# Performance work log

Measured on AMD Instinct MI355X. Metric: run time of the kernel, lower is better.

The kernel has to match this reference:

```python
import jax, jax.numpy as jnp
import numpy as np

B, N, D = 512, 2048, 128
MASK_NEG = 1e30


def setup_inputs() -> dict:
    key = jax.random.key(0)
    ks = jax.random.split(key, 8)
    Q = jax.random.normal(ks[0], (B, D), dtype=jnp.float32)
    K = jax.random.normal(ks[1], (B, N, D), dtype=jnp.float32)
    V = jax.random.normal(ks[2], (B, N, D), dtype=jnp.float32)
    adj = jax.random.randint(ks[3], (B, N), 0, 2).astype(jnp.float32)  # 0/1 mask
    s_mask = jnp.zeros((B, N), dtype=jnp.int32)  # unused by forward, kept for fidelity
    # nn.Linear params (PyTorch default uniform init scale)
    bound = 1.0 / np.sqrt(D)
    W1 = jax.random.uniform(ks[4], (D, D), minval=-bound, maxval=bound, dtype=jnp.float32)
    b1 = jax.random.uniform(ks[5], (D,), minval=-bound, maxval=bound, dtype=jnp.float32)
    W2 = jax.random.uniform(ks[6], (D, D), minval=-bound, maxval=bound, dtype=jnp.float32)
    b2 = jax.random.uniform(ks[7], (D,), minval=-bound, maxval=bound, dtype=jnp.float32)
    return {"Q": Q, "K": K, "V": V, "adj": adj, "s_mask": s_mask,
            "W1": W1, "b1": b1, "W2": W2, "b2": b2}


def reference(Q, K, V, adj, s_mask, W1, b1, W2, b2):
    # linear1(Q): (B, D); linear2(K): (B, N, D)  (torch Linear: x @ W.T + b)
    Qp = Q @ W1.T + b1
    Kp = jnp.einsum('bnd,de->bne', K, W2.T) + b2
    # bmm(K, Q.unsqueeze(2)).permute -> (B, 1, N) attention logits
    alpha = jnp.einsum('bnd,bd->bn', Kp, Qp)
    alpha = alpha - (1.0 - adj) * 1e30  # mask_logic with adj
    attn_weight = jax.nn.softmax(alpha, axis=-1)  # (B, N)
    attn_sum = jnp.einsum('bn,bnd->bd', attn_weight, V)  # (B, D)
    return attn_weight[:, None, :], attn_sum
```

## Files before the change

kernel.cpp:

```cpp
#include <hip/hip_runtime.h>
#include <cmath>

#define BB 512
#define NN 2048
#define DD 128

__global__ __launch_bounds__(128) void prep_kernel(
    const float* __restrict__ Q, const float* __restrict__ W1,
    const float* __restrict__ b1, const float* __restrict__ W2,
    const float* __restrict__ b2, float* __restrict__ qt,
    float* __restrict__ cvec) {
  const int b = blockIdx.x;
  const int t = threadIdx.x;
  __shared__ float Qs[DD];
  __shared__ float Qp[DD];
  __shared__ float red[DD];

  Qs[t] = Q[b * DD + t];
  __syncthreads();

  float acc = b1[t];
  const float4* w1row = (const float4*)(W1 + t * DD);
  #pragma unroll 8
  for (int i = 0; i < DD / 4; ++i) {
    float4 w = w1row[i];
    acc += Qs[4 * i + 0] * w.x + Qs[4 * i + 1] * w.y +
           Qs[4 * i + 2] * w.z + Qs[4 * i + 3] * w.w;
  }
  Qp[t] = acc;
  __syncthreads();

  float acc2 = 0.f;
  for (int e = 0; e < DD; ++e) acc2 += Qp[e] * W2[e * DD + t];
  qt[b * DD + t] = acc2;

  red[t] = Qp[t] * b2[t];
  __syncthreads();
  for (int s = 64; s > 0; s >>= 1) {
    if (t < s) red[t] += red[t + s];
    __syncthreads();
  }
  if (t == 0) cvec[b] = red[0];
}

__global__ __launch_bounds__(256) void attn_kernel(
    const float* __restrict__ K, const float* __restrict__ V,
    const float* __restrict__ adj, const float* __restrict__ qt,
    const float* __restrict__ cvec, float* __restrict__ out_w,
    float* __restrict__ out_s) {
  const int b = blockIdx.x;
  const int tid = threadIdx.x;
  const int sub = tid & 31;
  const int grp = tid >> 5;

  __shared__ float alpha[NN];
  __shared__ float redC[8 * DD];
  __shared__ float wredM[4];
  __shared__ float wredS[4];

  const float4 qv = ((const float4*)(qt + (size_t)b * DD))[sub];
  const float cb = cvec[b];
  const float4* K4 = (const float4*)(K + (size_t)b * NN * DD);
  const float4* V4 = (const float4*)(V + (size_t)b * NN * DD);
  const float* adjb = adj + (size_t)b * NN;

  for (int nb = grp * 4; nb < NN; nb += 32) {
    float4 k0 = K4[(nb + 0) * 32 + sub];
    float4 k1 = K4[(nb + 1) * 32 + sub];
    float4 k2 = K4[(nb + 2) * 32 + sub];
    float4 k3 = K4[(nb + 3) * 32 + sub];
    float p0 = k0.x * qv.x + k0.y * qv.y + k0.z * qv.z + k0.w * qv.w;
    float p1 = k1.x * qv.x + k1.y * qv.y + k1.z * qv.z + k1.w * qv.w;
    float p2 = k2.x * qv.x + k2.y * qv.y + k2.z * qv.z + k2.w * qv.w;
    float p3 = k3.x * qv.x + k3.y * qv.y + k3.z * qv.z + k3.w * qv.w;
    #pragma unroll
    for (int off = 16; off > 0; off >>= 1) {
      p0 += __shfl_xor(p0, off);
      p1 += __shfl_xor(p1, off);
      p2 += __shfl_xor(p2, off);
      p3 += __shfl_xor(p3, off);
    }
    if (sub == 0) {
      alpha[nb + 0] = p0 + cb - (1.0f - adjb[nb + 0]) * 1e30f;
      alpha[nb + 1] = p1 + cb - (1.0f - adjb[nb + 1]) * 1e30f;
      alpha[nb + 2] = p2 + cb - (1.0f - adjb[nb + 2]) * 1e30f;
      alpha[nb + 3] = p3 + cb - (1.0f - adjb[nb + 3]) * 1e30f;
    }
  }
  __syncthreads();

  float m = -INFINITY;
  for (int i = tid; i < NN; i += 256) m = fmaxf(m, alpha[i]);
  #pragma unroll
  for (int off = 32; off > 0; off >>= 1) m = fmaxf(m, __shfl_xor(m, off));
  if ((tid & 63) == 0) wredM[tid >> 6] = m;
  __syncthreads();
  m = fmaxf(fmaxf(wredM[0], wredM[1]), fmaxf(wredM[2], wredM[3]));

  float s = 0.f;
  for (int i = tid; i < NN; i += 256) {
    float p = __expf(alpha[i] - m);
    alpha[i] = p;
    s += p;
  }
  #pragma unroll
  for (int off = 32; off > 0; off >>= 1) s += __shfl_xor(s, off);
  if ((tid & 63) == 0) wredS[tid >> 6] = s;
  __syncthreads();
  s = wredS[0] + wredS[1] + wredS[2] + wredS[3];
  const float inv = 1.0f / s;

  for (int i = tid; i < NN; i += 256) {
    float w = alpha[i] * inv;
    alpha[i] = w;
    out_w[(size_t)b * NN + i] = w;
  }
  __syncthreads();

  float ax = 0.f, ay = 0.f, az = 0.f, aw = 0.f;
  for (int nb = grp * 4; nb < NN; nb += 32) {
    float w0 = alpha[nb + 0];
    float w1 = alpha[nb + 1];
    float w2 = alpha[nb + 2];
    float w3 = alpha[nb + 3];
    float4 v0 = V4[(nb + 0) * 32 + sub];
    float4 v1 = V4[(nb + 1) * 32 + sub];
    float4 v2 = V4[(nb + 2) * 32 + sub];
    float4 v3 = V4[(nb + 3) * 32 + sub];
    ax += w0 * v0.x + w1 * v1.x + w2 * v2.x + w3 * v3.x;
    ay += w0 * v0.y + w1 * v1.y + w2 * v2.y + w3 * v3.y;
    az += w0 * v0.z + w1 * v1.z + w2 * v2.z + w3 * v3.z;
    aw += w0 * v0.w + w1 * v1.w + w2 * v2.w + w3 * v3.w;
  }
  float4 accv;
  accv.x = ax; accv.y = ay; accv.z = az; accv.w = aw;
  ((float4*)redC)[grp * 32 + sub] = accv;
  __syncthreads();
  if (tid < DD) {
    float ssum = 0.f;
    #pragma unroll
    for (int g = 0; g < 8; ++g) ssum += redC[g * DD + tid];
    out_s[(size_t)b * DD + tid] = ssum;
  }
}

extern "C" void kernel_launch(void* const* d_in, const int* in_sizes, int n_in,
                              void* d_out, int out_size, void* d_ws, size_t ws_size,
                              hipStream_t stream) {
  const float* Q   = (const float*)d_in[0];
  const float* K   = (const float*)d_in[1];
  const float* V   = (const float*)d_in[2];
  const float* adj = (const float*)d_in[3];
  const float* W1  = (const float*)d_in[5];
  const float* b1  = (const float*)d_in[6];
  const float* W2  = (const float*)d_in[7];
  const float* b2  = (const float*)d_in[8];

  float* out_w = (float*)d_out;
  float* out_s = out_w + (size_t)BB * NN;

  float* qt   = (float*)d_ws;
  float* cvec = qt + (size_t)BB * DD;

  prep_kernel<<<BB, DD, 0, stream>>>(Q, W1, b1, W2, b2, qt, cvec);
  attn_kernel<<<BB, 256, 0, stream>>>(K, V, adj, qt, cvec, out_w, out_s);
}
```

Before: 996.1 us.

## Split attention over sequence chunks with flash-style softmax combine kernel

Splits each batch row's N dimension into 4 chunks, so 2048 blocks instead of 512 each compute local max, exp-sum and a partial V accumulation. A new combine kernel rescales the partials and the unnormalised weights with the global softmax factors. This raises parallelism and memory-level concurrency on a bandwidth-bound kernel. The cost is an extra launch and an extra read/write pass over out_w, and each warp has fewer loads in flight because the per-iteration unroll drops from 4 rows to 2.

```diff
diff --git a/kernel.cpp b/kernel.cpp
--- a/kernel.cpp
+++ b/kernel.cpp
@@ -4,6 +4,8 @@
 #define BB 512
 #define NN 2048
 #define DD 128
+#define SPLIT 4
+#define NC (NN / SPLIT)
 
 __global__ __launch_bounds__(128) void prep_kernel(
     const float* __restrict__ Q, const float* __restrict__ W1,
@@ -43,54 +45,49 @@
   if (t == 0) cvec[b] = red[0];
 }
 
-__global__ __launch_bounds__(256) void attn_kernel(
+__global__ __launch_bounds__(256, 8) void attn_part_kernel(
     const float* __restrict__ K, const float* __restrict__ V,
     const float* __restrict__ adj, const float* __restrict__ qt,
     const float* __restrict__ cvec, float* __restrict__ out_w,
-    float* __restrict__ out_s) {
+    float* __restrict__ part, float* __restrict__ mloc,
+    float* __restrict__ sloc) {
   const int b = blockIdx.x;
+  const int sc = blockIdx.y;
+  const int n0 = sc * NC;
   const int tid = threadIdx.x;
   const int sub = tid & 31;
   const int grp = tid >> 5;
 
-  __shared__ float alpha[NN];
+  __shared__ float alpha[NC];
   __shared__ float redC[8 * DD];
   __shared__ float wredM[4];
   __shared__ float wredS[4];
 
   const float4 qv = ((const float4*)(qt + (size_t)b * DD))[sub];
   const float cb = cvec[b];
-  const float4* K4 = (const float4*)(K + (size_t)b * NN * DD);
-  const float4* V4 = (const float4*)(V + (size_t)b * NN * DD);
-  const float* adjb = adj + (size_t)b * NN;
-
-  for (int nb = grp * 4; nb < NN; nb += 32) {
+  const float4* K4 = (const float4*)(K + ((size_t)b * NN + n0) * DD);
+  const float4* V4 = (const float4*)(V + ((size_t)b * NN + n0) * DD);
+  const float* adjb = adj + (size_t)b * NN + n0;
+
+  for (int nb = grp * 2; nb < NC; nb += 16) {
     float4 k0 = K4[(nb + 0) * 32 + sub];
     float4 k1 = K4[(nb + 1) * 32 + sub];
-    float4 k2 = K4[(nb + 2) * 32 + sub];
-    float4 k3 = K4[(nb + 3) * 32 + sub];
     float p0 = k0.x * qv.x + k0.y * qv.y + k0.z * qv.z + k0.w * qv.w;
     float p1 = k1.x * qv.x + k1.y * qv.y + k1.z * qv.z + k1.w * qv.w;
-    float p2 = k2.x * qv.x + k2.y * qv.y + k2.z * qv.z + k2.w * qv.w;
-    float p3 = k3.x * qv.x + k3.y * qv.y + k3.z * qv.z + k3.w * qv.w;
     #pragma unroll
     for (int off = 16; off > 0; off >>= 1) {
       p0 += __shfl_xor(p0, off);
       p1 += __shfl_xor(p1, off);
-      p2 += __shfl_xor(p2, off);
-      p3 += __shfl_xor(p3, off);
     }
     if (sub == 0) {
       alpha[nb + 0] = p0 + cb - (1.0f - adjb[nb + 0]) * 1e30f;
       alpha[nb + 1] = p1 + cb - (1.0f - adjb[nb + 1]) * 1e30f;
-      alpha[nb + 2] = p2 + cb - (1.0f - adjb[nb + 2]) * 1e30f;
-      alpha[nb + 3] = p3 + cb - (1.0f - adjb[nb + 3]) * 1e30f;
     }
   }
   __syncthreads();
 
   float m = -INFINITY;
-  for (int i = tid; i < NN; i += 256) m = fmaxf(m, alpha[i]);
+  for (int i = tid; i < NC; i += 256) m = fmaxf(m, alpha[i]);
   #pragma unroll
   for (int off = 32; off > 0; off >>= 1) m = fmaxf(m, __shfl_xor(m, off));
   if ((tid & 63) == 0) wredM[tid >> 6] = m;
@@ -98,9 +95,10 @@
   m = fmaxf(fmaxf(wredM[0], wredM[1]), fmaxf(wredM[2], wredM[3]));
 
   float s = 0.f;
-  for (int i = tid; i < NN; i += 256) {
+  for (int i = tid; i < NC; i += 256) {
     float p = __expf(alpha[i] - m);
     alpha[i] = p;
+    out_w[(size_t)b * NN + n0 + i] = p;
     s += p;
   }
   #pragma unroll
@@ -108,39 +106,71 @@
   if ((tid & 63) == 0) wredS[tid >> 6] = s;
   __syncthreads();
   s = wredS[0] + wredS[1] + wredS[2] + wredS[3];
-  const float inv = 1.0f / s;
-
-  for (int i = tid; i < NN; i += 256) {
-    float w = alpha[i] * inv;
-    alpha[i] = w;
-    out_w[(size_t)b * NN + i] = w;
-  }
-  __syncthreads();
+  if (tid == 0) {
+    mloc[b * SPLIT + sc] = m;
+    sloc[b * SPLIT + sc] = s;
+  }
 
   float ax = 0.f, ay = 0.f, az = 0.f, aw = 0.f;
-  for (int nb = grp * 4; nb < NN; nb += 32) {
+  for (int nb = grp * 2; nb < NC; nb += 16) {
     float w0 = alpha[nb + 0];
     float w1 = alpha[nb + 1];
-    float w2 = alpha[nb + 2];
-    float w3 = alpha[nb + 3];
     float4 v0 = V4[(nb + 0) * 32 + sub];
     float4 v1 = V4[(nb + 1) * 32 + sub];
-    float4 v2 = V4[(nb + 2) * 32 + sub];
-    float4 v3 = V4[(nb + 3) * 32 + sub];
-    ax += w0 * v0.x + w1 * v1.x + w2 * v2.x + w3 * v3.x;
-    ay += w0 * v0.y + w1 * v1.y + w2 * v2.y + w3 * v3.y;
-    az += w0 * v0.z + w1 * v1.z + w2 * v2.z + w3 * v3.z;
-    aw += w0 * v0.w + w1 * v1.w + w2 * v2.w + w3 * v3.w;
+    ax += w0 * v0.x + w1 * v1.x;
+    ay += w0 * v0.y + w1 * v1.y;
+    az += w0 * v0.z + w1 * v1.z;
+    aw += w0 * v0.w + w1 * v1.w;
   }
   float4 accv;
   accv.x = ax; accv.y = ay; accv.z = az; accv.w = aw;
+  __syncthreads();
   ((float4*)redC)[grp * 32 + sub] = accv;
   __syncthreads();
   if (tid < DD) {
     float ssum = 0.f;
     #pragma unroll
     for (int g = 0; g < 8; ++g) ssum += redC[g * DD + tid];
-    out_s[(size_t)b * DD + tid] = ssum;
+    part[((size_t)b * SPLIT + sc) * DD + tid] = ssum;
+  }
+}
+
+__global__ __launch_bounds__(256) void combine_kernel(
+    const float* __restrict__ part, const float* __restrict__ mloc,
+    const float* __restrict__ sloc, float* __restrict__ out_w,
+    float* __restrict__ out_s) {
+  const int b = blockIdx.x;
+  const int tid = threadIdx.x;
+
+  float M = -INFINITY;
+  #pragma unroll
+  for (int sc = 0; sc < SPLIT; ++sc) M = fmaxf(M, mloc[b * SPLIT + sc]);
+  float f[SPLIT];
+  float T = 0.f;
+  #pragma unroll
+  for (int sc = 0; sc < SPLIT; ++sc) {
+    float e = __expf(mloc[b * SPLIT + sc] - M);
+    T += sloc[b * SPLIT + sc] * e;
+    f[sc] = e;
+  }
+  const float inv = 1.0f / T;
+  #pragma unroll
+  for (int sc = 0; sc < SPLIT; ++sc) f[sc] *= inv;
+
+  if (tid < DD) {
+    float acc = 0.f;
+    #pragma unroll
+    for (int sc = 0; sc < SPLIT; ++sc)
+      acc += part[((size_t)b * SPLIT + sc) * DD + tid] * f[sc];
+    out_s[(size_t)b * DD + tid] = acc;
+  }
+
+  float4* w4 = (float4*)(out_w + (size_t)b * NN);
+  for (int i = tid; i < NN / 4; i += 256) {
+    const float fs = f[i >> 7];
+    float4 v = w4[i];
+    v.x *= fs; v.y *= fs; v.z *= fs; v.w *= fs;
+    w4[i] = v;
   }
 }
 
@@ -161,7 +191,13 @@
 
   float* qt   = (float*)d_ws;
   float* cvec = qt + (size_t)BB * DD;
+  float* part = cvec + BB;
+  float* mloc = part + (size_t)BB * SPLIT * DD;
+  float* sloc = mloc + (size_t)BB * SPLIT;
 
   prep_kernel<<<BB, DD, 0, stream>>>(Q, W1, b1, W2, b2, qt, cvec);
-  attn_kernel<<<BB, 256, 0, stream>>>(K, V, adj, qt, cvec, out_w, out_s);
-}
+  dim3 grid2(BB, SPLIT);
+  attn_part_kernel<<<grid2, 256, 0, stream>>>(K, V, adj, qt, cvec, out_w,
+                                              part, mloc, sloc);
+  combine_kernel<<<BB, 256, 0, stream>>>(part, mloc, sloc, out_w, out_s);
+}
```

After: 1.005 ms. Within noise of the previous version (+0.8%).
